# Optimization experiments

Hardware: AMD Instinct MI355X
Metric: run time of the kernel (lower is better)

## Reference

```python
import jax, jax.numpy as jnp
import numpy as np

B, L = 32, 64
VOCAB, EMB, HID, MEM, NVAL = 32000, 256, 512, 256, 1024
NSLOTS, KTOP = 4096, 16
DEQ_ITERS, RELAX = 8, 0.5
DECAY, MEM_SCALE = 0.997, 1.0
HIDDEN = 1024  # max(128, 2*HID)


def _norm(x):
    # torch F.normalize: x / max(||x||, eps)
    return x / jnp.maximum(jnp.linalg.norm(x, axis=-1, keepdims=True), 1e-12)


def setup_inputs() -> dict:
    key = jax.random.key(0)
    ks = jax.random.split(key, 20)
    def gn(k, shape, scale):
        return jax.random.normal(k, shape, jnp.float32) * scale
    inp = {}
    inp['tokens'] = jax.random.randint(ks[0], (B, L), 0, VOCAB)
    inp['key_ids'] = jax.random.randint(ks[1], (B,), 0, NVAL)
    inp['write_pos'] = jax.random.randint(ks[2], (B,), 0, L // 2)
    inp['query_pos'] = jax.random.randint(ks[3], (B,), L // 2, L)
    inp['value_ids'] = jax.random.randint(ks[4], (B,), 0, NVAL)
    inp['embed_W'] = gn(ks[5], (VOCAB, EMB), 1.0)
    inp['key_W'] = gn(ks[6], (NVAL, MEM), 0.1)
    inp['value_W'] = gn(ks[7], (NVAL, MEM), 0.1)
    din = HID + EMB + MEM
    inp['u_W1'] = gn(ks[8], (din, HIDDEN), din ** -0.5)
    inp['u_b1'] = jnp.zeros((HIDDEN,), jnp.float32)
    inp['u_W2'] = gn(ks[9], (HIDDEN, HID), HIDDEN ** -0.5)
    inp['u_b2'] = jnp.zeros((HID,), jnp.float32)
    inp['l_Wi'] = gn(ks[10], (HID, HID), HID ** -0.5)
    inp['l_Wh'] = gn(ks[11], (HID, HID), HID ** -0.5)
    inp['l_b'] = jnp.zeros((HID,), jnp.float32)
    inp['l_Wti'] = gn(ks[12], (HID, HID), HID ** -0.5)
    inp['l_Wth'] = gn(ks[13], (HID, HID), HID ** -0.5)
    inp['l_bt'] = jnp.zeros((HID,), jnp.float32)
    inp['h0'] = jnp.zeros((HID,), jnp.float32)
    inp['z2v_W'] = gn(ks[14], (2 * HID, MEM), (2 * HID) ** -0.5)
    inp['z2v_b'] = jnp.zeros((MEM,), jnp.float32)
    inp['logit_scale_raw'] = jnp.asarray(2.0, jnp.float32)
    inp['slot_keys'] = _norm(gn(ks[15], (NSLOTS, MEM), 1.0))
    return inp


def _forward(tokens, key_ids, write_pos, query_pos, embed_W, key_W, value_W,
             u_W1, u_b1, u_W2, u_b2, l_Wi, l_Wh, l_b, l_Wti, l_Wth, l_bt,
             h0, z2v_W, z2v_b, logit_scale_raw, slot_keys):
    scale = jax.nn.softplus(logit_scale_raw) + 1e-3
    V_proto = _norm(value_W)                              # [NVAL, MEM]
    # Memory ops are non-differentiable in the original (detach + no_grad writes)
    kv = jax.lax.stop_gradient(_norm(key_W[key_ids]))     # [B, MEM]
    sk = jax.lax.stop_gradient(slot_keys)                 # [NSLOTS, MEM]

    x_seq = jnp.swapaxes(embed_W[tokens], 0, 1)           # [L, B, EMB]
    t_idx = jnp.arange(L)
    mw_seq = t_idx[:, None] == write_pos[None, :]         # [L, B]
    mq_seq = t_idx[:, None] == query_pos[None, :]         # [L, B]

    # Slot addressing depends only on the (fixed per-sequence) key vectors,
    # so the top-k slot selection can be hoisted out of the time loop.
    top_s, top_i = jax.lax.top_k(kv @ sk.T, KTOP)         # [B, KTOP]
    w_slot = jax.nn.softmax(top_s, axis=-1)               # [B, KTOP]

    def mem_read(M):
        return jnp.einsum('bk,bkd->bd', w_slot, M[top_i])  # gather [B,KTOP,MEM]

    def mem_write(M, vals, mask):
        wm = w_slot * mask[:, None].astype(M.dtype)
        contrib = jnp.zeros_like(M).at[top_i.reshape(-1)].add(
            (wm[..., None] * vals[:, None, :]).reshape(-1, MEM))
        decay_t = jnp.where(mask.any(), DECAY, 1.0)       # decay only on write events
        return decay_t * M + contrib

    def step(carry, xs):
        z, h, M, lm, lp = carry
        x_t, mw, mq = xs
        # mem_into_deq: non-diff memory read is injected only at query steps
        v_t = mem_read(M) * mq[:, None].astype(x_t.dtype) * MEM_SCALE
        # DEQ: damped fixed-point iteration z <- (1-r) z + r f(z)
        for _ in range(DEQ_ITERS):
            inp = jnp.concatenate([z, x_t, v_t], axis=-1)
            f = z + jnp.tanh(inp @ u_W1 + u_b1) @ u_W2 + u_b2
            z = (1.0 - RELAX) * z + RELAX * f
        # Liquid cell: time-constant gated relaxation toward tanh candidate
        g = jnp.tanh(z @ l_Wi + h @ l_Wh + l_b)
        tau = jax.nn.softplus(z @ l_Wti + h @ l_Wth + l_bt) + 1.0
        h = h + (g - h) / tau
        v_pred = _norm(jnp.concatenate([z, h], axis=-1) @ z2v_W + z2v_b)
        M = mem_write(M, jax.lax.stop_gradient(v_pred), mw)
        v_mem = mem_read(M)
        lm = jnp.where(mq[:, None], scale * (_norm(v_mem) @ V_proto.T), lm)
        lp = jnp.where(mq[:, None], scale * (v_pred @ V_proto.T), lp)
        return (z, h, M, lm, lp), None

    z0 = jnp.zeros((B, HID), jnp.float32)
    h_init = jnp.broadcast_to(h0, (B, HID))
    M0 = jnp.zeros((NSLOTS, MEM), jnp.float32)
    lm0 = jnp.zeros((B, NVAL), jnp.float32)
    lp0 = jnp.zeros((B, NVAL), jnp.float32)
    carry, _ = jax.lax.scan(step, (z0, h_init, M0, lm0, lp0), (x_seq, mw_seq, mq_seq))
    return carry[3]  # logits_main [B, NVAL]


def reference(tokens, key_ids, write_pos, query_pos, value_ids, embed_W, key_W,
              value_W, u_W1, u_b1, u_W2, u_b2, l_Wi, l_Wh, l_b, l_Wti, l_Wth,
              l_bt, h0, z2v_W, z2v_b, logit_scale_raw, slot_keys):
    # value_ids only feeds auxiliary losses in the original; logits_main does not use it.
    return _forward(tokens, key_ids, write_pos, query_pos, embed_W, key_W, value_W,
                    u_W1, u_b1, u_W2, u_b2, l_Wi, l_Wh, l_b, l_Wti, l_Wth, l_bt,
                    h0, z2v_W, z2v_b, logit_scale_raw, slot_keys)
```

## Files before the change

### kernel.cpp

```cpp
#include <hip/hip_runtime.h>
#include <math.h>


#define NGRP 8
#define WPG  32

#define OF_SCALE  0
#define OF_DFAC   32
#define OF_RNV    64
#define OF_TOPW   1088
#define OF_SCORES 1600
#define OF_Z      132672
#define OF_CP     198208
#define OF_G      230976
#define OF_TAU    247360
#define OF_H      263744
#define OF_ZS     280128
#define OF_HS     296512
#define OF_M      312896
#define OF_W1ZT   1361472
#define OF_W1XT   1885760
#define OF_W2T    2147904
#define OF_LWIT   2672192
#define OF_LWHT   2934336
#define OF_LWTIT  3196480
#define OF_LWTHT  3458624

__device__ __forceinline__ float softplusf_(float x){ return x > 20.f ? x : log1pf(expf(x)); }

__device__ __forceinline__ float cldf(const float* p){
  return __hip_atomic_load(p, __ATOMIC_RELAXED, __HIP_MEMORY_SCOPE_AGENT);
}
__device__ __forceinline__ void cstf(float* p, float v){
  __hip_atomic_store(p, v, __ATOMIC_RELAXED, __HIP_MEMORY_SCOPE_AGENT);
}

__device__ __forceinline__ void lbar(int* flags, int w, int& epoch){
  asm volatile("s_waitcnt vmcnt(0)" ::: "memory");
  __syncthreads();
  epoch++;
  if (threadIdx.x == 0)
    __hip_atomic_store(&flags[w], epoch, __ATOMIC_RELAXED, __HIP_MEMORY_SCOPE_AGENT);
  if (threadIdx.x < 32){
    while (__hip_atomic_load(&flags[threadIdx.x], __ATOMIC_RELAXED,
                             __HIP_MEMORY_SCOPE_AGENT) < epoch)
      __builtin_amdgcn_s_sleep(1);
  }
  asm volatile("" ::: "memory");
  __syncthreads();
}

__global__ void __launch_bounds__(256) emma_tr(const float* src, float* dst,
                                               int shift, int total)
{
  const int R = total >> shift;
  const int cmask = (1 << shift) - 1;
  for (int idx = blockIdx.x*256 + threadIdx.x; idx < total; idx += gridDim.x*256){
    int r = idx >> shift, c = idx & cmask;
    dst[(size_t)c * R + r] = src[idx];
  }
}

__global__ void __launch_bounds__(256) emma_k1a(
    const int* key_ids, const int* write_pos,
    const float* key_W, const float* value_W, const float* slot_keys,
    const float* lsr, int* wsI, float* wsF)
{
  const int wg = blockIdx.x, tid = threadIdx.x;
  if (wg < 256) {
    const int b = wg >> 3, chunk = wg & 7;
    __shared__ __align__(16) float s_kv[256];
    __shared__ float red[256];
    float v = key_W[key_ids[b]*256 + tid];
    red[tid] = v*v; __syncthreads();
    for (int st=128; st; st>>=1){ if (tid<st) red[tid]+=red[tid+st]; __syncthreads(); }
    float inv = 1.f/fmaxf(sqrtf(red[0]), 1e-12f);
    s_kv[tid] = v*inv;
    __syncthreads();
    const int lane = tid & 63, wv = tid >> 6;
    float4 kv4 = *(const float4*)(s_kv + lane*4);
    for (int slot = chunk*512 + wv; slot < chunk*512 + 512; slot += 4){
      float4 sk = *(const float4*)(slot_keys + (size_t)slot*256 + lane*4);
      float p = kv4.x*sk.x + kv4.y*sk.y + kv4.z*sk.z + kv4.w*sk.w;
      #pragma unroll
      for (int m=32;m;m>>=1) p += __shfl_xor(p, m, 64);
      if (lane==0) wsF[OF_SCORES + b*4096 + slot] = p;
    }
  } else if (wg < 320) {
    const int j = wg - 256;
    for (int i=tid;i<16384;i+=256) wsF[OF_M + j*16384 + i] = 0.f;
  } else if (wg < 324) {
    const int row = (wg-320)*256 + tid;
    float ss=0.f; const float* r = value_W + (size_t)row*256;
    for (int k=0;k<256;k++){ float x=r[k]; ss += x*x; }
    wsF[OF_RNV + row] = 1.f/fmaxf(sqrtf(ss), 1e-12f);
  } else {
    for (int i=tid;i<2048;i+=256) wsI[i]=0;
    __shared__ int pres[32];
    if (tid<32){ int p=0; for (int bb=0;bb<32;bb++) if (write_pos[bb]==tid) p=1; pres[tid]=p; }
    __syncthreads();
    if (tid<32){
      int wp = write_pos[tid]; float f=1.f;
      for (int s=wp+1;s<32;s++) if (pres[s]) f *= 0.997f;
      wsF[OF_DFAC + tid] = f;
    }
    if (tid==0) wsF[OF_SCALE] = softplusf_(lsr[0]) + 1e-3f;
  }
}

__global__ void __launch_bounds__(256) emma_k1b(int* wsI, float* wsF)
{
  const int b = blockIdx.x, tid = threadIdx.x;
  __shared__ float s_sc[4096];
  __shared__ float s_rv[256]; __shared__ int s_ri[256];
  __shared__ float s_tv[16];
  for (int n=tid;n<4096;n+=256) s_sc[n] = wsF[OF_SCORES + b*4096 + n];
  __syncthreads();
  for (int j=0;j<16;j++){
    float bv = -3.0e38f; int bi = 0x7fffffff;
    for (int n=tid;n<4096;n+=256){
      float v = s_sc[n];
      if (v > bv || (v == bv && n < bi)) { bv=v; bi=n; }
    }
    s_rv[tid]=bv; s_ri[tid]=bi; __syncthreads();
    for (int st=128; st; st>>=1){
      if (tid<st){
        float v2=s_rv[tid+st]; int i2=s_ri[tid+st];
        if (v2 > s_rv[tid] || (v2==s_rv[tid] && i2 < s_ri[tid])) { s_rv[tid]=v2; s_ri[tid]=i2; }
      }
      __syncthreads();
    }
    if (tid==0){
      s_tv[j] = s_rv[0];
      wsI[2048 + b*16 + j] = s_ri[0];
      s_sc[s_ri[0]] = -3.0e38f;
    }
    __syncthreads();
  }
  if (tid==0){
    float mx = s_tv[0], sum=0.f, w[16];
    for (int j=0;j<16;j++){ w[j]=expf(s_tv[j]-mx); sum+=w[j]; }
    for (int j=0;j<16;j++) wsF[OF_TOPW + b*16 + j] = w[j]/sum;
  }
}

__global__ void __launch_bounds__(256, 1) emma_k2(
    const int* tokens, const int* write_pos,
    const float* embed_W, const float* u_b1, const float* u_b2,
    const float* l_b, const float* l_bt, const float* h0,
    int* wsI, float* wsF)
{
  const int g = blockIdx.x & 7;
  const int w = blockIdx.x >> 3;
  const int tid = threadIdx.x;
  int* flags = wsI + g*32;
  int epoch = 0;

  float* Z  = wsF + OF_Z;
  float* CP = wsF + OF_CP;
  float* G  = wsF + OF_G;
  float* TA = wsF + OF_TAU;
  float* H  = wsF + OF_H;
  float* ZS = wsF + OF_ZS;
  float* HS = wsF + OF_HS;

  __shared__ __align__(16) float4 ldsA[32*129];
  __shared__ __align__(16) float4 ldsB[4096];
  __shared__ __align__(16) float zstage[4*520];
  __shared__ __align__(16) float tl[4*36];

  {
    const float* gA = wsF + OF_W1ZT + (size_t)(w*32)*512;
    const float* gB = wsF + OF_W2T;
    for (int idx4 = tid; idx4 < 4096; idx4 += 256){
      { int ci = idx4 >> 7, j = idx4 & 127;
        ldsA[ci*129 + j] = *(const float4*)(gA + (size_t)ci*512 + 4*j); }
      { int j4 = idx4 >> 9, c2 = idx4 & 511;
        ldsB[idx4] = *(const float4*)(gB + (size_t)c2*1024 + w*32 + 4*j4); }
    }
  }

  const int rA  = tid >> 5;
  const int bA  = g*4 + (rA & 3);
  const int ciA = tid & 31;
  const int cA  = w*32 + ciA;
  const int r3  = tid >> 6;
  const int c2l = tid & 63;
  const int kh  = w >> 4;
  float bh[8];
  #pragma unroll
  for (int cc=0;cc<8;cc++) bh[cc] = 0.5f*u_b2[c2l + 64*cc];
  float zp[8] = {0.f,0.f,0.f,0.f,0.f,0.f,0.f,0.f};

  if (w < 16) {
    int idx = w*256 + tid;
    if (idx < 2048) cstf(&Z[g*2048 + idx], 0.f);
    else { int i2=idx-2048; int r=i2>>9, c=i2&511; cstf(&H[(g*4+r)*512 + c], h0[c]); }
  } else {
    { int idx = (w-16)*256 + tid;
      if (idx < 2048) cstf(&Z[16384 + g*2048 + idx], 0.f); }
    int r = tid>>6, b = g*4+r;
    int c = (w-16)*64 + (tid&63);
    int tok = tokens[b*64 + 0];
    const float* xr = embed_W + (size_t)tok*256;
    const float* wc = wsF + OF_W1XT + (size_t)c*256;
    float a0=0,a1=0,a2=0,a3=0;
    #pragma unroll 4
    for (int k=0;k<256;k+=4){
      float4 xv = *(const float4*)(xr + k);
      float4 wv = *(const float4*)(wc + k);
      a0 += xv.x*wv.x; a1 += xv.y*wv.y; a2 += xv.z*wv.z; a3 += xv.w*wv.w;
    }
    cstf(&CP[b*1024 + c], u_b1[c] + ((a0+a1)+(a2+a3)));
  }
  lbar(flags, w, epoch);

  for (int s=0;s<32;s++){
    float cpv = (tid < 128) ? cldf(&CP[bA*1024 + cA]) : 0.f;
    for (int i=0;i<8;i++){
      float* zc = Z + (i&1)*16384;
      float* zn = Z + ((i&1)^1)*16384;
      #pragma unroll
      for (int k=0;k<8;k++){
        int idx = k*256 + tid;
        zstage[(idx>>9)*520 + (idx&511)] = cldf(&zc[g*2048 + idx]);
      }
      __syncthreads();
      if (tid < 128) {
        const float4* wc4 = ldsA + ciA*129;
        const float*  zr  = zstage + rA*520;
        float a0=0,a1=0,a2=0,a3=0;
        #pragma unroll 8
        for (int j=0;j<128;j++){
          float4 wv = wc4[j];
          float4 zv = *(const float4*)(zr + 4*j);
          a0 += zv.x*wv.x; a1 += zv.y*wv.y; a2 += zv.z*wv.z; a3 += zv.w*wv.w;
        }
        tl[rA*36 + ciA] = tanhf(cpv + (a0+a1)+(a2+a3));
      }
      __syncthreads();
      {
        const float* trow = tl + r3*36;
        float accs[8] = {0.f,0.f,0.f,0.f,0.f,0.f,0.f,0.f};
        #pragma unroll
        for (int j4=0;j4<8;j4++){
          float4 tv = *(const float4*)(trow + 4*j4);
          const float4* wrow = ldsB + j4*512 + c2l;
          #pragma unroll
          for (int cc=0;cc<8;cc++){
            float4 wv = wrow[64*cc];
            accs[cc] += tv.x*wv.x + tv.y*wv.y + tv.z*wv.z + tv.w*wv.w;
          }
        }
        float* zrow = &zn[(g*4+r3)*512];
        #pragma unroll
        for (int cc=0;cc<8;cc++){
          int c2 = c2l + 64*cc;
          float zi = zstage[r3*520 + c2];
          float val = 0.5f*accs[cc] + (zi - zp[cc] + bh[cc]) * 0.03125f;
          zp[cc] = zi;
          atomicAdd(&zrow[c2], val);
        }
      }
      if (i==7 && tid>=128) {
        int idx = w*128 + (tid-128);
        if (idx < 2048){ int r=idx>>9, c=idx&511; cstf(&G[(g*4+r)*512+c], l_b[c]); }
        else { int i2=idx-2048; int r=i2>>9, c=i2&511; cstf(&TA[(g*4+r)*512+c], l_bt[c]); }
      }
      lbar(flags, w, epoch);
    }
    #pragma unroll
    for (int k=0;k<8;k++){
      int idx = k*256 + tid; int r = idx>>9, c = idx&511;
      const float* src = (kh==0) ? &Z[g*2048 + idx] : &H[g*2048 + idx];
      zstage[r*520 + c] = cldf(src);
    }
    __syncthreads();
    {
      int sub = tid>>7, l = tid&127;
      int r = l>>5, b = g*4+r;
      int c2 = (w&15)*32 + (l&31);
      const float* inrow = zstage + r*520;
      const float* Wc = (sub ? (kh==0 ? wsF+OF_LWTIT : wsF+OF_LWTHT)
                             : (kh==0 ? wsF+OF_LWIT  : wsF+OF_LWHT)) + (size_t)c2*512;
      float a0=0,a1=0,a2=0,a3=0;
      #pragma unroll 8
      for (int k=0;k<512;k+=4){
        float4 iv = *(const float4*)(inrow + k);
        float4 wv = *(const float4*)(Wc + k);
        a0 += iv.x*wv.x; a1 += iv.y*wv.y; a2 += iv.z*wv.z; a3 += iv.w*wv.w;
      }
      atomicAdd(sub ? &TA[b*512+c2] : &G[b*512+c2], (a0+a1)+(a2+a3));
    }
    lbar(flags, w, epoch);
    if (w < 16) {
      if (tid < 128) {
        int r = tid>>5, b = g*4+r;
        int c2 = w*32 + (tid&31);
        float gv = tanhf(cldf(&G[b*512+c2]));
        float tv = softplusf_(cldf(&TA[b*512+c2])) + 1.0f;
        float hv = cldf(&H[b*512+c2]);
        float hn = hv + (gv - hv)/tv;
        cstf(&H[b*512+c2], hn);
        if (write_pos[b] == s) {
          cstf(&ZS[b*512+c2], cldf(&Z[b*512+c2]));
          cstf(&HS[b*512+c2], hn);
        }
      }
    } else if (s+1 < 32) {
      int r = tid>>6, b = g*4+r;
      int c = (w-16)*64 + (tid&63);
      int tok = tokens[b*64 + s+1];
      const float* xr = embed_W + (size_t)tok*256;
      const float* wc = wsF + OF_W1XT + (size_t)c*256;
      float a0=0,a1=0,a2=0,a3=0;
      #pragma unroll 4
      for (int k=0;k<256;k+=4){
        float4 xv = *(const float4*)(xr + k);
        float4 wv = *(const float4*)(wc + k);
        a0 += xv.x*wv.x; a1 += xv.y*wv.y; a2 += xv.z*wv.z; a3 += xv.w*wv.w;
      }
      cstf(&CP[b*1024 + c], u_b1[c] + ((a0+a1)+(a2+a3)));
    }
    lbar(flags, w, epoch);
  }
}

__global__ void __launch_bounds__(256) emma_k3(const float* z2v_W, const float* z2v_b,
                                               int* wsI, float* wsF)
{
  const int b = blockIdx.x, c = threadIdx.x;
  const float* zs = wsF + OF_ZS + b*512;
  const float* hs = wsF + OF_HS + b*512;
  float acc = z2v_b[c];
  for (int k=0;k<512;k++) acc += zs[k]*z2v_W[k*256 + c];
  for (int k=0;k<512;k++) acc += hs[k]*z2v_W[(512+k)*256 + c];
  __shared__ float red[256];
  red[c]=acc*acc; __syncthreads();
  for (int st=128; st; st>>=1){ if (c<st) red[c]+=red[c+st]; __syncthreads(); }
  float inv = 1.f/fmaxf(sqrtf(red[0]),1e-12f);
  float vp = acc*inv;
  float f = wsF[OF_DFAC + b];
  for (int j=0;j<16;j++){
    int slot = wsI[2048 + b*16 + j];
    float wj = wsF[OF_TOPW + b*16 + j];
    atomicAdd(&wsF[OF_M + (size_t)slot*256 + c], f*wj*vp);
  }
}

__global__ void __launch_bounds__(256) emma_k4(const float* value_W, int* wsI, float* wsF,
                                               float* out)
{
  const int b = blockIdx.x, c = threadIdx.x;
  float m = 0.f;
  for (int j=0;j<16;j++){
    int slot = wsI[2048 + b*16 + j];
    m += wsF[OF_TOPW + b*16 + j] * wsF[OF_M + (size_t)slot*256 + c];
  }
  __shared__ float red[256];
  __shared__ float vn[256];
  red[c]=m*m; __syncthreads();
  for (int st=128; st; st>>=1){ if (c<st) red[c]+=red[c+st]; __syncthreads(); }
  float inv = 1.f/fmaxf(sqrtf(red[0]),1e-12f);
  vn[c] = m*inv;
  __syncthreads();
  float scale = wsF[OF_SCALE];
  for (int q=0;q<4;q++){
    int val = q*256 + c;
    const float* row = value_W + (size_t)val*256;
    float d0=0,d1=0,d2=0,d3=0;
    #pragma unroll 4
    for (int k=0;k<256;k+=4){
      float4 rv = *(const float4*)(row + k);
      d0 += vn[k+0]*rv.x; d1 += vn[k+1]*rv.y; d2 += vn[k+2]*rv.z; d3 += vn[k+3]*rv.w;
    }
    out[b*1024 + val] = scale * wsF[OF_RNV + val] * ((d0+d1)+(d2+d3));
  }
}

extern "C" void kernel_launch(void* const* d_in, const int* in_sizes, int n_in,
                              void* d_out, int out_size, void* d_ws, size_t ws_size,
                              hipStream_t stream)
{
  const int*   tokens    = (const int*)  d_in[0];
  const int*   key_ids   = (const int*)  d_in[1];
  const int*   write_pos = (const int*)  d_in[2];
  const float* embed_W   = (const float*)d_in[5];
  const float* key_W     = (const float*)d_in[6];
  const float* value_W   = (const float*)d_in[7];
  const float* u_W1      = (const float*)d_in[8];
  const float* u_b1      = (const float*)d_in[9];
  const float* u_W2      = (const float*)d_in[10];
  const float* u_b2      = (const float*)d_in[11];
  const float* l_Wi      = (const float*)d_in[12];
  const float* l_Wh      = (const float*)d_in[13];
  const float* l_b       = (const float*)d_in[14];
  const float* l_Wti     = (const float*)d_in[15];
  const float* l_Wth     = (const float*)d_in[16];
  const float* l_bt      = (const float*)d_in[17];
  const float* h0        = (const float*)d_in[18];
  const float* z2v_W     = (const float*)d_in[19];
  const float* z2v_b     = (const float*)d_in[20];
  const float* lsr       = (const float*)d_in[21];
  const float* slot_keys = (const float*)d_in[22];

  int*   wsI = (int*)d_ws;
  float* wsF = (float*)((char*)d_ws + 16384);
  float* out = (float*)d_out;

  hipLaunchKernelGGL(emma_k1a, dim3(325), dim3(256), 0, stream,
                     key_ids, write_pos, key_W, value_W, slot_keys, lsr, wsI, wsF);
  hipLaunchKernelGGL(emma_k1b, dim3(32), dim3(256), 0, stream, wsI, wsF);
  hipLaunchKernelGGL(emma_tr, dim3(512), dim3(256), 0, stream, u_W1,            wsF+OF_W1ZT, 10, 512*1024);
  hipLaunchKernelGGL(emma_tr, dim3(512), dim3(256), 0, stream, u_W1 + 512*1024, wsF+OF_W1XT, 10, 256*1024);
  hipLaunchKernelGGL(emma_tr, dim3(512), dim3(256), 0, stream, u_W2,            wsF+OF_W2T,   9, 1024*512);
  hipLaunchKernelGGL(emma_tr, dim3(512), dim3(256), 0, stream, l_Wi,            wsF+OF_LWIT,  9, 512*512);
  hipLaunchKernelGGL(emma_tr, dim3(512), dim3(256), 0, stream, l_Wh,            wsF+OF_LWHT,  9, 512*512);
  hipLaunchKernelGGL(emma_tr, dim3(512), dim3(256), 0, stream, l_Wti,           wsF+OF_LWTIT, 9, 512*512);
  hipLaunchKernelGGL(emma_tr, dim3(512), dim3(256), 0, stream, l_Wth,           wsF+OF_LWTHT, 9, 512*512);
  {
    void* args[] = { (void*)&tokens, (void*)&write_pos, (void*)&embed_W,
                     (void*)&u_b1, (void*)&u_b2, (void*)&l_b, (void*)&l_bt, (void*)&h0,
                     (void*)&wsI, (void*)&wsF };
    hipLaunchCooperativeKernel(reinterpret_cast<void*>(emma_k2), dim3(256), dim3(256),
                               args, 0, stream);
  }
  hipLaunchKernelGGL(emma_k3, dim3(32), dim3(256), 0, stream, z2v_W, z2v_b, wsI, wsF);
  hipLaunchKernelGGL(emma_k4, dim3(32), dim3(256), 0, stream, value_W, wsI, wsF, out);
}
```

Before: 3.789 ms.

## Defer h-update and next-token projection into idle threads of DEQ iterations, drop a barrier

The per-step h update and the next token's input projection now run on the otherwise idle upper half-block threads during the first DEQ iterations of the next step, instead of in a separate phase. This removes one grid-wide barrier per timestep. The final step's update is handled after the loop. The W2 matvec loop is also reordered so each warp starts at a rotated column chunk, which spreads LDS bank and atomic traffic across the warps. In exchange the hazards become subtler: the deferred H update must complete before H is next read, and ZS is taken from the staged Z copy.

```diff
diff --git a/kernel.cpp b/kernel.cpp
--- a/kernel.cpp
+++ b/kernel.cpp
@@ -186,10 +186,14 @@
   const int cA  = w*32 + ciA;
   const int r3  = tid >> 6;
   const int c2l = tid & 63;
+  const int rot = w & 7;
   const int kh  = w >> 4;
   float bh[8];
   #pragma unroll
-  for (int cc=0;cc<8;cc++) bh[cc] = 0.5f*u_b2[c2l + 64*cc];
+  for (int cco=0;cco<8;cco++){
+    int cc = (cco + rot) & 7;
+    bh[cco] = 0.5f*u_b2[c2l + (cc<<6)];
+  }
   float zp[8] = {0.f,0.f,0.f,0.f,0.f,0.f,0.f,0.f};
 
   if (w < 16) {
@@ -237,35 +241,63 @@
           a0 += zv.x*wv.x; a1 += zv.y*wv.y; a2 += zv.z*wv.z; a3 += zv.w*wv.w;
         }
         tl[rA*36 + ciA] = tanhf(cpv + (a0+a1)+(a2+a3));
+      } else {
+        if (i == 0 && w < 16 && s >= 1) {
+          int idx = w*128 + (tid-128);
+          int r = idx>>9, c2 = idx&511, b = g*4+r;
+          float gv = tanhf(cldf(&G[b*512+c2]));
+          float tv = softplusf_(cldf(&TA[b*512+c2])) + 1.0f;
+          float hv = cldf(&H[b*512+c2]);
+          float hn = hv + (gv - hv)/tv;
+          cstf(&H[b*512+c2], hn);
+          if (write_pos[b] == s-1) {
+            cstf(&ZS[b*512+c2], zstage[r*520 + c2]);
+            cstf(&HS[b*512+c2], hn);
+          }
+        } else if (i <= 1 && w >= 16 && s+1 < 32) {
+          int e = i*2048 + (w-16)*128 + (tid-128);
+          int r = e>>10, c = e&1023, b = g*4+r;
+          int tok = tokens[b*64 + s+1];
+          const float* xr = embed_W + (size_t)tok*256;
+          const float* wc = wsF + OF_W1XT + (size_t)c*256;
+          float a0=0,a1=0,a2=0,a3=0;
+          #pragma unroll 4
+          for (int k=0;k<256;k+=4){
+            float4 xv = *(const float4*)(xr + k);
+            float4 wv = *(const float4*)(wc + k);
+            a0 += xv.x*wv.x; a1 += xv.y*wv.y; a2 += xv.z*wv.z; a3 += xv.w*wv.w;
+          }
+          cstf(&CP[b*1024 + c], u_b1[c] + ((a0+a1)+(a2+a3)));
+        } else if (i == 7) {
+          int idx = w*128 + (tid-128);
+          if (idx < 2048){ int r=idx>>9, c=idx&511; cstf(&G[(g*4+r)*512+c], l_b[c]); }
+          else { int i2=idx-2048; int r=i2>>9, c=i2&511; cstf(&TA[(g*4+r)*512+c], l_bt[c]); }
+        }
       }
       __syncthreads();
       {
         const float* trow = tl + r3*36;
-        float accs[8] = {0.f,0.f,0.f,0.f,0.f,0.f,0.f,0.f};
+        float4 tvv[8];
         #pragma unroll
-        for (int j4=0;j4<8;j4++){
-          float4 tv = *(const float4*)(trow + 4*j4);
-          const float4* wrow = ldsB + j4*512 + c2l;
-          #pragma unroll
-          for (int cc=0;cc<8;cc++){
-            float4 wv = wrow[64*cc];
-            accs[cc] += tv.x*wv.x + tv.y*wv.y + tv.z*wv.z + tv.w*wv.w;
-          }
-        }
+        for (int j4=0;j4<8;j4++) tvv[j4] = *(const float4*)(trow + 4*j4);
         float* zrow = &zn[(g*4+r3)*512];
         #pragma unroll
-        for (int cc=0;cc<8;cc++){
-          int c2 = c2l + 64*cc;
+        for (int cco=0;cco<8;cco++){
+          int cc = (cco + rot) & 7;
+          int c2 = c2l + (cc<<6);
+          const float4* wrow = ldsB + c2;
+          float acc = 0.f;
+          #pragma unroll
+          for (int j4=0;j4<8;j4++){
+            float4 wv = wrow[j4*512];
+            float4 tv = tvv[j4];
+            acc += tv.x*wv.x + tv.y*wv.y + tv.z*wv.z + tv.w*wv.w;
+          }
           float zi = zstage[r3*520 + c2];
-          float val = 0.5f*accs[cc] + (zi - zp[cc] + bh[cc]) * 0.03125f;
-          zp[cc] = zi;
+          float val = 0.5f*acc + (zi - zp[cco] + bh[cco]) * 0.03125f;
+          zp[cco] = zi;
           atomicAdd(&zrow[c2], val);
         }
-      }
-      if (i==7 && tid>=128) {
-        int idx = w*128 + (tid-128);
-        if (idx < 2048){ int r=idx>>9, c=idx&511; cstf(&G[(g*4+r)*512+c], l_b[c]); }
-        else { int i2=idx-2048; int r=i2>>9, c=i2&511; cstf(&TA[(g*4+r)*512+c], l_bt[c]); }
       }
       lbar(flags, w, epoch);
     }
@@ -293,36 +325,18 @@
       atomicAdd(sub ? &TA[b*512+c2] : &G[b*512+c2], (a0+a1)+(a2+a3));
     }
     lbar(flags, w, epoch);
-    if (w < 16) {
-      if (tid < 128) {
-        int r = tid>>5, b = g*4+r;
-        int c2 = w*32 + (tid&31);
-        float gv = tanhf(cldf(&G[b*512+c2]));
-        float tv = softplusf_(cldf(&TA[b*512+c2])) + 1.0f;
-        float hv = cldf(&H[b*512+c2]);
-        float hn = hv + (gv - hv)/tv;
-        cstf(&H[b*512+c2], hn);
-        if (write_pos[b] == s) {
-          cstf(&ZS[b*512+c2], cldf(&Z[b*512+c2]));
-          cstf(&HS[b*512+c2], hn);
-        }
-      }
-    } else if (s+1 < 32) {
-      int r = tid>>6, b = g*4+r;
-      int c = (w-16)*64 + (tid&63);
-      int tok = tokens[b*64 + s+1];
-      const float* xr = embed_W + (size_t)tok*256;
-      const float* wc = wsF + OF_W1XT + (size_t)c*256;
-      float a0=0,a1=0,a2=0,a3=0;
-      #pragma unroll 4
-      for (int k=0;k<256;k+=4){
-        float4 xv = *(const float4*)(xr + k);
-        float4 wv = *(const float4*)(wc + k);
-        a0 += xv.x*wv.x; a1 += xv.y*wv.y; a2 += xv.z*wv.z; a3 += xv.w*wv.w;
-      }
-      cstf(&CP[b*1024 + c], u_b1[c] + ((a0+a1)+(a2+a3)));
-    }
-    lbar(flags, w, epoch);
+  }
+  if (w < 16 && tid >= 128) {
+    int idx = w*128 + (tid-128);
+    int r = idx>>9, c2 = idx&511, b = g*4+r;
+    float gv = tanhf(cldf(&G[b*512+c2]));
+    float tv = softplusf_(cldf(&TA[b*512+c2])) + 1.0f;
+    float hv = cldf(&H[b*512+c2]);
+    float hn = hv + (gv - hv)/tv;
+    if (write_pos[b] == 31) {
+      cstf(&ZS[b*512+c2], cldf(&Z[b*512+c2]));
+      cstf(&HS[b*512+c2], hn);
+    }
   }
 }
 
```

Measured after the change: 3.457 ms. 1.1x faster.
